# Optimization experiments

Hardware: AMD Instinct MI355X
Metric: run time of the kernel (lower is better)

The kernel has to match this reference:

```python
import jax, jax.numpy as jnp
import numpy as np

B, L, D = 4, 4096, 1024
DI = 4 * D          # ff_expansion * embedding_dim
M = 8               # thought_memory_size
STEPS = 4           # num_thought_steps
THR = 0.5           # uncertainty_threshold
EPS = 1e-6          # LayerNorm epsilon


def _ln(x, g, b):
    m = jnp.mean(x, axis=-1, keepdims=True)
    v = jnp.mean(jnp.square(x - m), axis=-1, keepdims=True)
    return (x - m) * jax.lax.rsqrt(v + EPS) * g + b


def setup_inputs() -> dict:
    key = jax.random.key(0)
    ks = jax.random.split(key, 8)

    def glorot(k, shape):
        lim = np.sqrt(6.0 / (shape[0] + shape[1]))
        return jax.random.uniform(k, shape, jnp.float32, -lim, lim)

    return {
        "x": jax.random.normal(ks[0], (B, L, D), jnp.float32),
        "g1": jnp.ones((D,), jnp.float32),
        "b1": jnp.zeros((D,), jnp.float32),
        "W_up": glorot(ks[1], (D, DI)),
        "b_up": jnp.zeros((DI,), jnp.float32),
        "W_down": glorot(ks[2], (DI, D)),
        "b_down": jnp.zeros((D,), jnp.float32),
        "W_halt": glorot(ks[3], (D, 1)),
        "b_halt": jnp.zeros((1,), jnp.float32),
        "W_comp": glorot(ks[4], (D, M)),
        "b_comp": jnp.zeros((M,), jnp.float32),
        "W_attn": glorot(ks[5], (D, D)),
        "b_attn": jnp.zeros((D,), jnp.float32),
        "g2": jnp.ones((D,), jnp.float32),
        "b2": jnp.zeros((D,), jnp.float32),
    }


def reference(x, g1, b1, W_up, b_up, W_down, b_down, W_halt, b_halt,
              W_comp, b_comp, W_attn, b_attn, g2, b2):
    log_d = jnp.log(jnp.asarray(x.shape[-1], x.dtype))
    hidden = x
    cum = jnp.zeros(x.shape[:2] + (1,), x.dtype)   # cumulative halting mass [B,L,1]
    acc = jnp.zeros_like(x)                         # ACT-weighted output accumulator
    for _ in range(STEPS):
        # single thought step: pre-LN FFN with residual
        n = _ln(hidden, g1, b1)
        h_new = hidden + (jax.nn.gelu(n @ W_up + b_up, approximate=False) @ W_down + b_down)
        # thought memory: compress sequence into M slots, cross-attend back
        scores = h_new @ W_comp + b_comp                                   # [B,L,M]
        memory = jnp.einsum('blm,bld->bmd', jax.nn.softmax(scores, axis=1), h_new)  # [B,M,D]
        ctx = jnp.einsum('blm,bmd->bld', jax.nn.softmax(scores, axis=-1), memory)   # [B,L,D]
        h_new = h_new + ctx @ W_attn + b_attn
        # entropy-guided gating: only update uncertain positions
        logp = jax.nn.log_softmax(hidden, axis=-1)
        ent = -jnp.sum(jnp.exp(logp) * logp, axis=-1, keepdims=True) / log_d  # normalized entropy [B,L,1]
        h_new = jnp.where(ent > THR, h_new, hidden)
        # ACT-lite halting accumulation
        p = jax.nn.sigmoid(h_new @ W_halt + b_halt)   # [B,L,1]
        w = p * (1.0 - cum)
        acc = acc + w * h_new
        cum = cum + w
        hidden = h_new
    out = acc + (1.0 - cum) * hidden
    return _ln(out, g2, b2)
```

## Files before the change

kernel.cpp:

```cpp
#include <hip/hip_runtime.h>
#include <math.h>

#define Bn 4
#define Ln 4096
#define Dn 1024
#define DIn 4096
#define Mn 8
#define Rn (Bn*Ln)
#define CHUNK 4096
#define NCH (Rn/CHUNK)
#define NSTEP 4
#define THRc 0.5f
#define EPSc 1e-6f
#define LCH 32
#define LSUB (Ln/LCH)

typedef unsigned short bfu;
typedef _Float16 f16;
typedef __attribute__((ext_vector_type(8))) _Float16 f16x8;
typedef __attribute__((ext_vector_type(4))) _Float16 f16x4;
typedef __attribute__((ext_vector_type(4))) float f32x4;

__device__ __forceinline__ bfu f2b(float f) {
    union { float f; unsigned i; } v; v.f = f;
    unsigned r = v.i + 0x7FFFu + ((v.i >> 16) & 1u);
    return (bfu)(r >> 16);
}
__device__ __forceinline__ float b2f(bfu u) {
    union { float f; unsigned i; } v; v.i = ((unsigned)u) << 16; return v.f;
}

__device__ __forceinline__ float bsum(float v, float* sb) {
    #pragma unroll
    for (int off = 32; off; off >>= 1) v += __shfl_down(v, off);
    int wave = threadIdx.x >> 6, lane = threadIdx.x & 63;
    if (lane == 0) sb[wave] = v;
    __syncthreads();
    float r = sb[0] + sb[1] + sb[2] + sb[3];
    __syncthreads();
    return r;
}

__device__ __forceinline__ float bmax(float v, float* sb) {
    #pragma unroll
    for (int off = 32; off; off >>= 1) v = fmaxf(v, __shfl_down(v, off));
    int wave = threadIdx.x >> 6, lane = threadIdx.x & 63;
    if (lane == 0) sb[wave] = v;
    __syncthreads();
    float r = fmaxf(fmaxf(sb[0], sb[1]), fmaxf(sb[2], sb[3]));
    __syncthreads();
    return r;
}

__global__ __launch_bounds__(256)
void init_kernel(const float* __restrict__ x, float* __restrict__ hidden,
                 bfu* __restrict__ acc, float* __restrict__ cum) {
    size_t i = (size_t)blockIdx.x * 256 + threadIdx.x;
    float4 v = ((const float4*)x)[i];
    ((float4*)hidden)[i] = v;
    ushort4 z = {0, 0, 0, 0};
    *(ushort4*)(acc + i * 4) = z;
    if (i < Rn) cum[i] = 0.f;
}

__global__ __launch_bounds__(256)
void transpose_cvt_kernel(const float* __restrict__ W, f16* __restrict__ Wh,
                          int K, int N) {
    __shared__ float tile[32][33];
    int k0 = blockIdx.y * 32, n0 = blockIdx.x * 32;
    int t = threadIdx.x;
    int r = t >> 5, c = t & 31;
    #pragma unroll
    for (int j = 0; j < 4; j++)
        tile[r + j * 8][c] = W[(size_t)(k0 + r + j * 8) * N + n0 + c];
    __syncthreads();
    #pragma unroll
    for (int j = 0; j < 4; j++) {
        float v = tile[c][r + j * 8];
        size_t idx = (size_t)(n0 + r + j * 8) * K + k0 + c;
        Wh[idx] = (f16)v;
    }
}

__global__ __launch_bounds__(256)
void ln_ent_kernel(const float* __restrict__ hidden,
                   const float* __restrict__ g1, const float* __restrict__ b1,
                   f16* __restrict__ nh, float* __restrict__ ent_out) {
    __shared__ float sb[4];
    int row = blockIdx.x;
    int t = threadIdx.x;
    const float* h = hidden + (size_t)row * Dn;
    float4 hv = ((const float4*)h)[t];
    float vals[4] = {hv.x, hv.y, hv.z, hv.w};
    float s = 0.f, s2 = 0.f, mx = -INFINITY;
    #pragma unroll
    for (int i = 0; i < 4; i++) { s += vals[i]; s2 += vals[i]*vals[i]; mx = fmaxf(mx, vals[i]); }
    s  = bsum(s,  sb);
    s2 = bsum(s2, sb);
    mx = bmax(mx, sb);
    float mean = s * (1.f / Dn);
    float var  = s2 * (1.f / Dn) - mean * mean;
    float rstd = rsqrtf(var + EPSc);
    float Z = 0.f, S = 0.f;
    #pragma unroll
    for (int i = 0; i < 4; i++) { float e = expf(vals[i] - mx); Z += e; S += e * vals[i]; }
    Z = bsum(Z, sb);
    S = bsum(S, sb);
    if (t == 0) {
        ent_out[row] = (mx + logf(Z) - S / Z) * (1.0f / logf((float)Dn));
    }
    float4 g = ((const float4*)g1)[t];
    float4 bb = ((const float4*)b1)[t];
    f16x4 oh;
    oh[0] = (f16)((vals[0] - mean) * rstd * g.x + bb.x);
    oh[1] = (f16)((vals[1] - mean) * rstd * g.y + bb.y);
    oh[2] = (f16)((vals[2] - mean) * rstd * g.z + bb.z);
    oh[3] = (f16)((vals[3] - mean) * rstd * g.w + bb.w);
    *(f16x4*)(nh + (size_t)row * Dn + t * 4) = oh;
}

template<int MODE>
__global__ __launch_bounds__(256, 4)
void gemm_f16(const f16* __restrict__ A, const f16* __restrict__ Bt,
              const float* __restrict__ bias, const float* __restrict__ res,
              void* __restrict__ C0, float* __restrict__ part,
              int N, int LD, int KLEN) {
    constexpr int MF = 4, NF = 4;
    __shared__ __align__(16) f16 sA[2][128 * 32];
    __shared__ __align__(16) f16 sB[2][128 * 32];
    int tid = threadIdx.x;
    int wave = tid >> 6, lane = tid & 63;
    int wm = wave >> 1, wn = wave & 1;
    int quad = lane >> 4, l15 = lane & 15;

    int nwg = gridDim.x * gridDim.y;
    int bid = blockIdx.y * gridDim.x + blockIdx.x;
    int swz = (bid & 7) * (nwg >> 3) + (bid >> 3);
    int bx = swz % gridDim.x, by = swz / gridDim.x;
    int m0 = by * 128, n0 = bx * 128;
    int kbase = blockIdx.z * KLEN;

    f32x4 acc[MF][NF];
    #pragma unroll
    for (int i = 0; i < MF; i++)
        #pragma unroll
        for (int j = 0; j < NF; j++)
            acc[i][j] = (f32x4){0.f, 0.f, 0.f, 0.f};

    int swzcol = ((lane & 3) ^ ((lane >> 3) & 3)) * 8;
    size_t aoff = (size_t)(m0 + wave * 32 + (lane >> 2)) * LD + kbase + swzcol;
    size_t boff = (size_t)(n0 + wave * 32 + (lane >> 2)) * LD + kbase + swzcol;
    const f16* gA = A + aoff;
    const f16* gB = Bt + boff;
    const int lA = wave * 1024;
    const int swzrd = (quad ^ ((l15 >> 1) & 3)) * 8;

    #define GLL(g, l) __builtin_amdgcn_global_load_lds( \
        (const __attribute__((address_space(1))) void*)(g), \
        (__attribute__((address_space(3))) void*)(l), 16, 0, 0)

    #define STAGE(BUF, KT) do { \
        size_t _ko = (size_t)(KT) * 32; \
        _Pragma("unroll") \
        for (int i = 0; i < 2; i++) { \
            GLL(gA + _ko + (size_t)i * 16 * LD, &sA[BUF][lA + i * 512]); \
            GLL(gB + _ko + (size_t)i * 16 * LD, &sB[BUF][lA + i * 512]); \
        } \
    } while (0)

    #define COMPUTE(BUF) do { \
        f16x8 af[MF], bf[NF]; \
        _Pragma("unroll") \
        for (int mt = 0; mt < MF; mt++) \
            af[mt] = *(const f16x8*)&sA[BUF][(wm * 64 + mt * 16 + l15) * 32 + swzrd]; \
        _Pragma("unroll") \
        for (int nt = 0; nt < NF; nt++) \
            bf[nt] = *(const f16x8*)&sB[BUF][(wn * 64 + nt * 16 + l15) * 32 + swzrd]; \
        _Pragma("unroll") \
        for (int mt = 0; mt < MF; mt++) \
            _Pragma("unroll") \
            for (int nt = 0; nt < NF; nt++) \
                acc[mt][nt] = __builtin_amdgcn_mfma_f32_16x16x32_f16(af[mt], bf[nt], acc[mt][nt], 0, 0, 0); \
    } while (0)

    const int nk = KLEN / 32;
    STAGE(0, 0);
    __syncthreads();
    int t = 0;
    for (; t < nk - 1; ++t) {
        STAGE((t + 1) & 1, t + 1);
        COMPUTE(t & 1);
        __syncthreads();
    }
    COMPUTE(t & 1);
    #undef STAGE
    #undef COMPUTE
    #undef GLL

    #pragma unroll
    for (int nt = 0; nt < NF; nt++) {
        int gcol = n0 + wn * 64 + nt * 16 + l15;
        float bv = (MODE == 0 || blockIdx.z == 0) ? bias[gcol] : 0.f;
        #pragma unroll
        for (int mt = 0; mt < MF; mt++) {
            int grow = m0 + wm * 64 + mt * 16 + quad * 4;
            #pragma unroll
            for (int r = 0; r < 4; r++) {
                size_t off = (size_t)(grow + r) * N + gcol;
                float v = acc[mt][nt][r] + bv;
                if (MODE == 0) {
                    v = 0.5f * v * (1.0f + erff(v * 0.70710678118654752f));
                    ((f16*)C0)[off] = (f16)v;
                } else {
                    if (blockIdx.z == 0) ((float*)C0)[off] = res[off] + v;
                    else                 part[off] = v;
                }
            }
        }
    }
}

__global__ __launch_bounds__(256)
void add_kernel(float* __restrict__ h, const float* __restrict__ p) {
    size_t i = (size_t)blockIdx.x * 256 + threadIdx.x;
    float4 a = ((float4*)h)[i];
    float4 b = ((const float4*)p)[i];
    a.x += b.x; a.y += b.y; a.z += b.z; a.w += b.w;
    ((float4*)h)[i] = a;
}

__global__ __launch_bounds__(256)
void scores_kernel(const float* __restrict__ h, const float* __restrict__ Wc,
                   const float* __restrict__ bc, float* __restrict__ scores) {
    int row = blockIdx.x;
    int t = threadIdx.x;
    float acc[Mn] = {};
    const float* hr = h + (size_t)row * Dn;
    for (int d = t; d < Dn; d += 256) {
        float hv = hr[d];
        const float* w = Wc + (size_t)d * Mn;
        #pragma unroll
        for (int m = 0; m < Mn; m++) acc[m] += hv * w[m];
    }
    __shared__ float red[Mn][4];
    int wave = t >> 6, lane = t & 63;
    #pragma unroll
    for (int m = 0; m < Mn; m++) {
        float v = acc[m];
        #pragma unroll
        for (int off = 32; off; off >>= 1) v += __shfl_down(v, off);
        if (lane == 0) red[m][wave] = v;
    }
    __syncthreads();
    if (t < Mn) {
        float v = red[t][0] + red[t][1] + red[t][2] + red[t][3];
        scores[(size_t)row * Mn + t] = v + bc[t];
    }
}

__global__ __launch_bounds__(256)
void softmaxL_kernel(const float* __restrict__ scores, float* __restrict__ wL) {
    __shared__ float sb[4];
    int b = blockIdx.x / Mn, m = blockIdx.x % Mn;
    int t = threadIdx.x;
    const float* s = scores + (size_t)b * Ln * Mn + m;
    float mx = -INFINITY;
    for (int l = t; l < Ln; l += 256) mx = fmaxf(mx, s[(size_t)l * Mn]);
    mx = bmax(mx, sb);
    float z = 0.f;
    for (int l = t; l < Ln; l += 256) z += expf(s[(size_t)l * Mn] - mx);
    z = bsum(z, sb);
    float inv = 1.0f / z;
    float* w = wL + (size_t)b * Ln * Mn + m;
    for (int l = t; l < Ln; l += 256) w[(size_t)l * Mn] = expf(s[(size_t)l * Mn] - mx) * inv;
}

__global__ __launch_bounds__(256)
void memory_kernel(const float* __restrict__ h, const float* __restrict__ wL,
                   float* __restrict__ mpart) {
    int bid = blockIdx.x;
    int lc = bid & (LCH - 1);
    int dc = (bid >> 5) & 3;
    int b  = bid >> 7;
    int t = threadIdx.x;
    int d = dc * 256 + t;
    int l0 = lc * LSUB;
    float acc[Mn] = {};
    const float* hp = h + ((size_t)b * Ln + l0) * Dn + d;
    const float* wp = wL + ((size_t)b * Ln + l0) * Mn;
    for (int l = 0; l < LSUB; l++) {
        float hv = hp[(size_t)l * Dn];
        float4 w0 = *(const float4*)(wp + (size_t)l * Mn);
        float4 w1 = *(const float4*)(wp + (size_t)l * Mn + 4);
        acc[0] += w0.x * hv; acc[1] += w0.y * hv; acc[2] += w0.z * hv; acc[3] += w0.w * hv;
        acc[4] += w1.x * hv; acc[5] += w1.y * hv; acc[6] += w1.z * hv; acc[7] += w1.w * hv;
    }
    #pragma unroll
    for (int m = 0; m < Mn; m++)
        mpart[(((size_t)lc * Bn + b) * Mn + m) * Dn + d] = acc[m];
}

__global__ __launch_bounds__(256)
void memreduce_kernel(const float* __restrict__ mpart, float* __restrict__ mem) {
    int i = blockIdx.x * 256 + threadIdx.x;
    float s = 0.f;
    #pragma unroll
    for (int lc = 0; lc < LCH; lc++) s += mpart[(size_t)lc * Bn * Mn * Dn + i];
    mem[i] = s;
}

__global__ __launch_bounds__(256)
void memw_kernel(const float* __restrict__ mem, const float* __restrict__ W,
                 float* __restrict__ memW) {
    __shared__ float sm[Dn];
    int bm = blockIdx.x >> 2;
    int dc = (blockIdx.x & 3) * 256;
    int t = threadIdx.x;
    const float* mrow = mem + (size_t)bm * Dn;
    for (int k = t; k < Dn; k += 256) sm[k] = mrow[k];
    __syncthreads();
    int d = dc + t;
    float a = 0.f;
    for (int k = 0; k < Dn; k++)
        a += sm[k] * W[(size_t)k * Dn + d];
    memW[(size_t)bm * Dn + d] = a;
}

__global__ __launch_bounds__(256)
void ctx_gate_kernel(const float* __restrict__ scores, const float* __restrict__ memW,
                     const float* __restrict__ battn, const float* __restrict__ hnew,
                     float* __restrict__ hidden, const float* __restrict__ ent,
                     const float* __restrict__ Wh, const float* __restrict__ bh,
                     bfu* __restrict__ acc, float* __restrict__ cum) {
    __shared__ float sb[4];
    int row = blockIdx.x;
    int b = row >> 12;
    int t = threadIdx.x;
    bool upd = ent[row] > THRc;
    float4 hv;
    if (upd) {
        const float* s = scores + (size_t)row * Mn;
        float sv[Mn];
        float mx = -INFINITY;
        #pragma unroll
        for (int m = 0; m < Mn; m++) { sv[m] = s[m]; mx = fmaxf(mx, sv[m]); }
        float z = 0.f;
        #pragma unroll
        for (int m = 0; m < Mn; m++) { sv[m] = expf(sv[m] - mx); z += sv[m]; }
        float inv = 1.0f / z;
        float4 bv = ((const float4*)battn)[t];
        float a0 = bv.x, a1 = bv.y, a2 = bv.z, a3 = bv.w;
        #pragma unroll
        for (int m = 0; m < Mn; m++) {
            float w = sv[m] * inv;
            float4 mw = ((const float4*)(memW + ((size_t)b * Mn + m) * Dn))[t];
            a0 += w * mw.x; a1 += w * mw.y; a2 += w * mw.z; a3 += w * mw.w;
        }
        hv = ((const float4*)(hnew + (size_t)row * Dn))[t];
        hv.x += a0; hv.y += a1; hv.z += a2; hv.w += a3;
    } else {
        hv = ((const float4*)(hidden + (size_t)row * Dn))[t];
    }
    float4 wv = ((const float4*)Wh)[t];
    float dot = hv.x*wv.x + hv.y*wv.y + hv.z*wv.z + hv.w*wv.w;
    dot = bsum(dot, sb);
    float p = 1.0f / (1.0f + expf(-(dot + bh[0])));
    float c = cum[row];
    float w = p * (1.0f - c);
    ushort4 a = *(ushort4*)(acc + (size_t)row * Dn + t * 4);
    ushort4 o;
    o.x = f2b(b2f(a.x) + w * hv.x);
    o.y = f2b(b2f(a.y) + w * hv.y);
    o.z = f2b(b2f(a.z) + w * hv.z);
    o.w = f2b(b2f(a.w) + w * hv.w);
    *(ushort4*)(acc + (size_t)row * Dn + t * 4) = o;
    ((float4*)(hidden + (size_t)row * Dn))[t] = hv;
    __syncthreads();
    if (t == 0) cum[row] = c + w;
}

__global__ __launch_bounds__(256)
void final_ln_kernel(const bfu* __restrict__ acc, const float* __restrict__ cum,
                     const float* __restrict__ hidden,
                     const float* __restrict__ g2, const float* __restrict__ b2,
                     float* __restrict__ out) {
    __shared__ float sb[4];
    int row = blockIdx.x;
    int t = threadIdx.x;
    float c = 1.0f - cum[row];
    ushort4 a = *(const ushort4*)(acc + (size_t)row * Dn + t * 4);
    float4 h = ((const float4*)(hidden + (size_t)row * Dn))[t];
    float vals[4];
    vals[0] = b2f(a.x) + c * h.x; vals[1] = b2f(a.y) + c * h.y;
    vals[2] = b2f(a.z) + c * h.z; vals[3] = b2f(a.w) + c * h.w;
    float s = 0.f, s2 = 0.f;
    #pragma unroll
    for (int i = 0; i < 4; i++) { s += vals[i]; s2 += vals[i]*vals[i]; }
    s  = bsum(s,  sb);
    s2 = bsum(s2, sb);
    float mean = s * (1.f / Dn);
    float var  = s2 * (1.f / Dn) - mean * mean;
    float rstd = rsqrtf(var + EPSc);
    float4 g = ((const float4*)g2)[t];
    float4 bb = ((const float4*)b2)[t];
    float4 o;
    o.x = (vals[0] - mean) * rstd * g.x + bb.x;
    o.y = (vals[1] - mean) * rstd * g.y + bb.y;
    o.z = (vals[2] - mean) * rstd * g.z + bb.z;
    o.w = (vals[3] - mean) * rstd * g.w + bb.w;
    ((float4*)(out + (size_t)row * Dn))[t] = o;
}

extern "C" void kernel_launch(void* const* d_in, const int* in_sizes, int n_in,
                              void* d_out, int out_size, void* d_ws, size_t ws_size,
                              hipStream_t stream) {
    (void)in_sizes; (void)n_in; (void)out_size; (void)ws_size;
    const float* x      = (const float*)d_in[0];
    const float* g1     = (const float*)d_in[1];
    const float* b1     = (const float*)d_in[2];
    const float* W_up   = (const float*)d_in[3];
    const float* b_up   = (const float*)d_in[4];
    const float* W_down = (const float*)d_in[5];
    const float* b_down = (const float*)d_in[6];
    const float* W_halt = (const float*)d_in[7];
    const float* b_halt = (const float*)d_in[8];
    const float* W_comp = (const float*)d_in[9];
    const float* b_comp = (const float*)d_in[10];
    const float* W_attn = (const float*)d_in[11];
    const float* b_attn = (const float*)d_in[12];
    const float* g2     = (const float*)d_in[13];
    const float* b2     = (const float*)d_in[14];
    float* out = (float*)d_out;

    char* wsb = (char*)d_ws;
    size_t off = 0;
    float* hidden = (float*)(wsb + off); off += (size_t)Rn * Dn * 4;
    float* hnew   = (float*)(wsb + off); off += (size_t)Rn * Dn * 4;
    bfu*   accb   = (bfu*)  (wsb + off); off += (size_t)Rn * Dn * 2;
    f16*   nh     = (f16*)  (wsb + off); off += (size_t)CHUNK * Dn * 2;
    f16*   uh     = (f16*)  (wsb + off); off += (size_t)CHUNK * DIn * 2;
    float* p1     = (float*)(wsb + off); off += (size_t)CHUNK * Dn * 4;
    f16*   WupTh  = (f16*)  (wsb + off); off += (size_t)DIn * Dn * 2;
    f16*   WdnTh  = (f16*)  (wsb + off); off += (size_t)Dn * DIn * 2;
    float* scores = (float*)(wsb + off); off += (size_t)Rn * Mn * 4;
    float* wL     = (float*)(wsb + off); off += (size_t)Rn * Mn * 4;
    float* mpart  = (float*)(wsb + off); off += (size_t)LCH * Bn * Mn * Dn * 4;
    float* memb   = (float*)(wsb + off); off += (size_t)Bn * Mn * Dn * 4;
    float* memW   = (float*)(wsb + off); off += (size_t)Bn * Mn * Dn * 4;
    float* ent    = (float*)(wsb + off); off += (size_t)Rn * 4;
    float* cum    = (float*)(wsb + off); off += (size_t)Rn * 4;

    transpose_cvt_kernel<<<dim3(DIn / 32, Dn / 32), 256, 0, stream>>>(W_up,   WupTh, Dn, DIn);
    transpose_cvt_kernel<<<dim3(Dn / 32, DIn / 32), 256, 0, stream>>>(W_down, WdnTh, DIn, Dn);

    init_kernel<<<(Rn * Dn / 4) / 256, 256, 0, stream>>>(x, hidden, accb, cum);

    for (int s = 0; s < NSTEP; ++s) {
        for (int c = 0; c < NCH; ++c) {
            ln_ent_kernel<<<CHUNK, 256, 0, stream>>>(
                hidden + (size_t)c * CHUNK * Dn, g1, b1, nh, ent + (size_t)c * CHUNK);
            gemm_f16<0><<<dim3(DIn / 128, CHUNK / 128, 1), 256, 0, stream>>>(
                nh, WupTh, b_up, nullptr, uh, nullptr, DIn, Dn, Dn);
            gemm_f16<1><<<dim3(Dn / 128, CHUNK / 128, 2), 256, 0, stream>>>(
                uh, WdnTh, b_down, hidden + (size_t)c * CHUNK * Dn,
                hnew + (size_t)c * CHUNK * Dn, p1, Dn, DIn, DIn / 2);
            add_kernel<<<(CHUNK * Dn / 4) / 256, 256, 0, stream>>>(
                hnew + (size_t)c * CHUNK * Dn, p1);
        }
        scores_kernel<<<Rn, 256, 0, stream>>>(hnew, W_comp, b_comp, scores);
        softmaxL_kernel<<<Bn * Mn, 256, 0, stream>>>(scores, wL);
        memory_kernel<<<Bn * (Dn / 256) * LCH, 256, 0, stream>>>(hnew, wL, mpart);
        memreduce_kernel<<<(Bn * Mn * Dn) / 256, 256, 0, stream>>>(mpart, memb);
        memw_kernel<<<Bn * Mn * 4, 256, 0, stream>>>(memb, W_attn, memW);
        ctx_gate_kernel<<<Rn, 256, 0, stream>>>(scores, memW, b_attn, hnew, hidden,
                                                ent, W_halt, b_halt, accb, cum);
    }

    final_ln_kernel<<<Rn, 256, 0, stream>>>(accb, cum, hidden, g2, b2, out);
}
```

Baseline: 2.841 ms.

## Split down-projection K four ways with fp16 partials and explicit vmcnt pipelining

Raises the split-K factor of the down-projection GEMM from 2 to 4, so the grid fills more of the GPU, and stores the three non-primary partial sums in fp16 in separate buffers. The add kernel then sums all three. The GEMM main loop replaces __syncthreads with a raw s_barrier plus an explicit s_waitcnt vmcnt(4), so the next tile's global loads can stay in flight during compute. In exchange the partials lose precision, there is extra partial traffic, and the fixed vmcnt value assumes a particular count of outstanding loads per STAGE.

```diff
diff --git a/kernel.cpp b/kernel.cpp
--- a/kernel.cpp
+++ b/kernel.cpp
@@ -30,6 +30,15 @@
     union { float f; unsigned i; } v; v.i = ((unsigned)u) << 16; return v.f;
 }
 
+template<int N>
+__device__ __forceinline__ void waitv() {
+    asm volatile("s_waitcnt vmcnt(%0)" :: "i"(N) : "memory");
+}
+__device__ __forceinline__ void block_bar() {
+    __builtin_amdgcn_s_barrier();
+    __builtin_amdgcn_sched_barrier(0);
+}
+
 __device__ __forceinline__ float bsum(float v, float* sb) {
     #pragma unroll
     for (int off = 32; off; off >>= 1) v += __shfl_down(v, off);
@@ -123,9 +132,10 @@
 __global__ __launch_bounds__(256, 4)
 void gemm_f16(const f16* __restrict__ A, const f16* __restrict__ Bt,
               const float* __restrict__ bias, const float* __restrict__ res,
-              void* __restrict__ C0, float* __restrict__ part,
+              void* __restrict__ C0, f16* __restrict__ part,
               int N, int LD, int KLEN) {
     constexpr int MF = 4, NF = 4;
+    constexpr int G  = 4;
     __shared__ __align__(16) f16 sA[2][128 * 32];
     __shared__ __align__(16) f16 sB[2][128 * 32];
     int tid = threadIdx.x;
@@ -185,18 +195,23 @@
 
     const int nk = KLEN / 32;
     STAGE(0, 0);
-    __syncthreads();
-    int t = 0;
-    for (; t < nk - 1; ++t) {
-        STAGE((t + 1) & 1, t + 1);
+    for (int t = 0; t < nk; ++t) {
+        if (t + 1 < nk) {
+            STAGE((t + 1) & 1, t + 1);
+            waitv<G>();
+        } else {
+            waitv<0>();
+        }
+        block_bar();
         COMPUTE(t & 1);
-        __syncthreads();
-    }
-    COMPUTE(t & 1);
+        block_bar();
+    }
     #undef STAGE
     #undef COMPUTE
     #undef GLL
 
+    f16* pp = (MODE == 1 && blockIdx.z > 0)
+              ? part + (size_t)(blockIdx.z - 1) * (size_t)gridDim.y * 128 * N : part;
     #pragma unroll
     for (int nt = 0; nt < NF; nt++) {
         int gcol = n0 + wn * 64 + nt * 16 + l15;
@@ -213,7 +228,7 @@
                     ((f16*)C0)[off] = (f16)v;
                 } else {
                     if (blockIdx.z == 0) ((float*)C0)[off] = res[off] + v;
-                    else                 part[off] = v;
+                    else                 pp[off] = (f16)v;
                 }
             }
         }
@@ -221,11 +236,16 @@
 }
 
 __global__ __launch_bounds__(256)
-void add_kernel(float* __restrict__ h, const float* __restrict__ p) {
+void add_kernel(float* __restrict__ h, const f16* __restrict__ p) {
     size_t i = (size_t)blockIdx.x * 256 + threadIdx.x;
     float4 a = ((float4*)h)[i];
-    float4 b = ((const float4*)p)[i];
-    a.x += b.x; a.y += b.y; a.z += b.z; a.w += b.w;
+    f16x4 q0 = ((const f16x4*)p)[i];
+    f16x4 q1 = ((const f16x4*)(p + (size_t)CHUNK * Dn))[i];
+    f16x4 q2 = ((const f16x4*)(p + (size_t)2 * CHUNK * Dn))[i];
+    a.x += (float)q0[0] + (float)q1[0] + (float)q2[0];
+    a.y += (float)q0[1] + (float)q1[1] + (float)q2[1];
+    a.z += (float)q0[2] + (float)q1[2] + (float)q2[2];
+    a.w += (float)q0[3] + (float)q1[3] + (float)q2[3];
     ((float4*)h)[i] = a;
 }
 
@@ -439,7 +459,7 @@
     bfu*   accb   = (bfu*)  (wsb + off); off += (size_t)Rn * Dn * 2;
     f16*   nh     = (f16*)  (wsb + off); off += (size_t)CHUNK * Dn * 2;
     f16*   uh     = (f16*)  (wsb + off); off += (size_t)CHUNK * DIn * 2;
-    float* p1     = (float*)(wsb + off); off += (size_t)CHUNK * Dn * 4;
+    f16*   pf     = (f16*)  (wsb + off); off += (size_t)3 * CHUNK * Dn * 2;
     f16*   WupTh  = (f16*)  (wsb + off); off += (size_t)DIn * Dn * 2;
     f16*   WdnTh  = (f16*)  (wsb + off); off += (size_t)Dn * DIn * 2;
     float* scores = (float*)(wsb + off); off += (size_t)Rn * Mn * 4;
@@ -461,11 +481,11 @@
                 hidden + (size_t)c * CHUNK * Dn, g1, b1, nh, ent + (size_t)c * CHUNK);
             gemm_f16<0><<<dim3(DIn / 128, CHUNK / 128, 1), 256, 0, stream>>>(
                 nh, WupTh, b_up, nullptr, uh, nullptr, DIn, Dn, Dn);
-            gemm_f16<1><<<dim3(Dn / 128, CHUNK / 128, 2), 256, 0, stream>>>(
+            gemm_f16<1><<<dim3(Dn / 128, CHUNK / 128, 4), 256, 0, stream>>>(
                 uh, WdnTh, b_down, hidden + (size_t)c * CHUNK * Dn,
-                hnew + (size_t)c * CHUNK * Dn, p1, Dn, DIn, DIn / 2);
+                hnew + (size_t)c * CHUNK * Dn, pf, Dn, DIn, DIn / 4);
             add_kernel<<<(CHUNK * Dn / 4) / 256, 256, 0, stream>>>(
-                hnew + (size_t)c * CHUNK * Dn, p1);
+                hnew + (size_t)c * CHUNK * Dn, pf);
         }
         scores_kernel<<<Rn, 256, 0, stream>>>(hnew, W_comp, b_comp, scores);
         softmaxL_kernel<<<Bn * Mn, 256, 0, stream>>>(scores, wL);
```

New measurement: 2.962 ms. 4.2% more time.
